# Kernel optimization log

Measured on AMD Instinct MI355X. Metric: run time of the kernel, lower is better.

The kernel has to match this reference:

```python
import jax, jax.numpy as jnp
import numpy as np

B, S = 64, 64
IMG_F, EMB, HID, VOCAB = 2048, 512, 512, 32000


def setup_inputs() -> dict:
    key = jax.random.key(0)
    ks = jax.random.split(key, 12)
    s = 0.02
    return {
        "img": jax.random.normal(ks[0], (B, IMG_F), jnp.float32),
        "captions": jax.random.randint(ks[1], (B, S), 0, VOCAB),
        "embed_W": jax.random.normal(ks[2], (VOCAB, EMB), jnp.float32) * s,
        "Wi": jax.random.normal(ks[3], (IMG_F, HID), jnp.float32) * s,
        "bi": jax.random.normal(ks[4], (HID,), jnp.float32) * s,
        "Wx": jax.random.normal(ks[5], (EMB, HID), jnp.float32) * s,
        "bx": jax.random.normal(ks[6], (HID,), jnp.float32) * s,
        "Wh": jax.random.normal(ks[7], (HID, HID), jnp.float32) * s,
        "bh": jax.random.normal(ks[8], (HID, HID)[:1] + (HID,), jnp.float32)[0] * s if False else jax.random.normal(ks[8], (HID,), jnp.float32) * s,
        "Wy": jax.random.normal(ks[9], (HID, VOCAB), jnp.float32) * s,
        "by": jax.random.normal(ks[10], (VOCAB,), jnp.float32) * s,
    }


def reference(img, captions, embed_W, Wi, bi, Wx, bx, Wh, bh, Wy, by):
    # Embed caption inputs (drop last token): (B, T, EMB), T = S-1
    x = embed_W[captions[:, :-1]]
    # Precompute input-to-hidden preactivations for all steps: (B, T, HID)
    pre = jnp.einsum("bte,eh->bth", x, Wx) + bx
    # Image features are injected only at t=0 (as in the torch loop)
    pre = pre.at[:, 0].add(img @ Wi + bi)

    def step(h_prev, p_t):
        h_t = jnp.tanh(p_t + h_prev @ Wh + bh)
        return h_t, h_t

    h0 = jnp.zeros((img.shape[0], Wh.shape[0]), dtype=x.dtype)
    _, hs = jax.lax.scan(step, h0, pre.transpose(1, 0, 2))  # (T, B, HID)
    hs = hs.transpose(1, 0, 2)  # (B, T, HID)
    # Output projection in one big GEMM (same math as per-step h2y)
    logits = jnp.einsum("bth,hv->btv", hs, Wy) + by  # (B, T, VOCAB)
    return logits
```

## Files before the change

kernel.cpp:

```cpp
#include <hip/hip_runtime.h>
#include <hip/hip_bf16.h>

#define B_    64
#define S_    64
#define T_    63
#define IMGF  2048
#define EMB   512
#define HID   512
#define VOCAB 32000
#define MROWS 4032
#define MPAD  4096

typedef __bf16 bf16;
typedef __bf16 bf16x8 __attribute__((ext_vector_type(8)));
typedef float  f32x4  __attribute__((ext_vector_type(4)));

__device__ __forceinline__ void gload_lds16(const void* g, void* l) {
  __builtin_amdgcn_global_load_lds(
      (const __attribute__((address_space(1))) unsigned int*)g,
      (__attribute__((address_space(3))) unsigned int*)l, 16, 0, 0);
}

__global__ __launch_bounds__(256) void transpose_w(
    const float* __restrict__ W, bf16* __restrict__ WT, int K, int N)
{
  __shared__ float tile[64][65];
  const int tx = threadIdx.x & 63, ty = threadIdx.x >> 6;
  const int n0 = blockIdx.x * 64, k0 = blockIdx.y * 64;
  #pragma unroll
  for (int r = ty; r < 64; r += 4)
    tile[r][tx] = W[(size_t)(k0 + r) * N + n0 + tx];
  __syncthreads();
  #pragma unroll
  for (int r = ty; r < 64; r += 4)
    WT[(size_t)(n0 + r) * K + k0 + tx] = (bf16)tile[tx][r];
}

__global__ __launch_bounds__(256) void embed_gather(
    const float* __restrict__ embW, const int* __restrict__ captions,
    bf16* __restrict__ X)
{
  const int r = blockIdx.x;
  const int tid = threadIdx.x;
  if (r < MROWS) {
    const int b = r / T_, t = r % T_;
    const int idx = captions[b * S_ + t];
    float2 v = ((const float2*)(embW + (size_t)idx * EMB))[tid];
    X[(size_t)r * EMB + 2 * tid]     = (bf16)v.x;
    X[(size_t)r * EMB + 2 * tid + 1] = (bf16)v.y;
  } else {
    X[(size_t)r * EMB + 2 * tid]     = (bf16)0.f;
    X[(size_t)r * EMB + 2 * tid + 1] = (bf16)0.f;
  }
}

__global__ __launch_bounds__(256) void img_to_bf16(
    const float* __restrict__ img, bf16* __restrict__ imgB)
{
  const int r = blockIdx.x;
  const int tid = threadIdx.x;
  #pragma unroll
  for (int j = 0; j < 8; j++) {
    const int c = tid + j * 256;
    const float v = (r < B_) ? img[(size_t)r * IMGF + c] : 0.f;
    imgB[(size_t)r * IMGF + c] = (bf16)v;
  }
}

__global__ __launch_bounds__(256) void gemm_bt(
    const bf16* __restrict__ A, const bf16* __restrict__ BT,
    const float* __restrict__ bias, float* __restrict__ C,
    int Mvalid, int N, int K)
{
  __shared__ __align__(16) bf16 As[128 * 32];
  __shared__ __align__(16) bf16 Bs[128 * 32];
  const int tid  = threadIdx.x;
  const int wave = tid >> 6, lane = tid & 63;
  const int wm = wave >> 1, wn = wave & 1;
  const int bn = blockIdx.x, bm = blockIdx.y;
  const int lg = lane >> 4, lr = lane & 15;

  f32x4 acc[4][4];
  #pragma unroll
  for (int m = 0; m < 4; m++)
    #pragma unroll
    for (int n = 0; n < 4; n++) acc[m][n] = (f32x4){0.f, 0.f, 0.f, 0.f};

  const bf16* Abase = A  + (size_t)bm * 128 * K;
  const bf16* Bbase = BT + (size_t)bn * 128 * K;

  for (int kt = 0; kt < K; kt += 32) {
    __syncthreads();
    #pragma unroll
    for (int i = 0; i < 2; i++) {
      const int c = i * 256 + wave * 64 + lane;
      const int r = c >> 2;
      const int sl = (c & 3) ^ ((r >> 1) & 3);
      gload_lds16(Abase + (size_t)r * K + kt + sl * 8,
                  &As[(i * 256 + wave * 64) * 8]);
    }
    #pragma unroll
    for (int i = 0; i < 2; i++) {
      const int c = i * 256 + wave * 64 + lane;
      const int r = c >> 2;
      const int sl = (c & 3) ^ ((r >> 1) & 3);
      gload_lds16(Bbase + (size_t)r * K + kt + sl * 8,
                  &Bs[(i * 256 + wave * 64) * 8]);
    }
    __syncthreads();

    bf16x8 af[4], bfr[4];
    #pragma unroll
    for (int m = 0; m < 4; m++) {
      const int r = wm * 64 + m * 16 + lr;
      const int sp = lg ^ ((r >> 1) & 3);
      af[m] = *(const bf16x8*)&As[r * 32 + sp * 8];
    }
    #pragma unroll
    for (int n = 0; n < 4; n++) {
      const int r = wn * 64 + n * 16 + lr;
      const int sp = lg ^ ((r >> 1) & 3);
      bfr[n] = *(const bf16x8*)&Bs[r * 32 + sp * 8];
    }
    #pragma unroll
    for (int m = 0; m < 4; m++)
      #pragma unroll
      for (int n = 0; n < 4; n++)
        acc[m][n] = __builtin_amdgcn_mfma_f32_16x16x32_bf16(af[m], bfr[n], acc[m][n], 0, 0, 0);
  }

  const int row0 = bm * 128 + wm * 64 + (lane >> 4) * 4;
  const int col0 = bn * 128 + wn * 64 + lr;
  #pragma unroll
  for (int m = 0; m < 4; m++) {
    #pragma unroll
    for (int n = 0; n < 4; n++) {
      const int col = col0 + n * 16;
      const float bv = bias[col];
      #pragma unroll
      for (int q = 0; q < 4; q++) {
        const int row = row0 + m * 16 + q;
        if (row < Mvalid) C[(size_t)row * N + col] = acc[m][n][q] + bv;
      }
    }
  }
}

#define FREG 47
#define FLDS 17
__global__ __launch_bounds__(512, 2) void rnn_reg8(
    const float* __restrict__ pre, const bf16* __restrict__ WhT,
    const float* __restrict__ bh, const float* __restrict__ pimg,
    bf16* __restrict__ hs)
{
  const int bg  = blockIdx.x;
  const int tid = threadIdx.x;
  const int wave = tid >> 6, lane = tid & 63;
  const int lg = lane >> 4, lr = lane & 15;
  const int gb0 = bg * 16;
  const int wc0 = wave * 64;

  __shared__ __align__(16) bf16 hsh[16 * 512];
  __shared__ __align__(16) bf16 bls[8 * FLDS * 64 * 8];

  bf16x8 bw[FREG];
  #pragma unroll
  for (int f = 0; f < 64; f++) {
    const int n = f >> 4, kf = f & 15;
    const bf16x8 v = *(const bf16x8*)(WhT + (size_t)(wc0 + n * 16 + lr) * 512
                                          + kf * 32 + lg * 8);
    if (f < FREG) bw[f] = v;
    else *(bf16x8*)&bls[((wave * FLDS + (f - FREG)) * 64 + lane) * 8] = v;
  }

  *(f32x4*)&hsh[tid * 16]     = (f32x4){0.f, 0.f, 0.f, 0.f};
  *(f32x4*)&hsh[tid * 16 + 8] = (f32x4){0.f, 0.f, 0.f, 0.f};

  float bhv[4];
  #pragma unroll
  for (int n = 0; n < 4; n++) bhv[n] = bh[wc0 + n * 16 + lr];
  const float* preb = pre + ((size_t)(gb0 + lg * 4) * T_) * 512 + wc0 + lr;

  __syncthreads();

  #pragma unroll 1
  for (int t = 0; t < T_; t++) {
    float prq[4][4];
    #pragma unroll
    for (int n = 0; n < 4; n++)
      #pragma unroll
      for (int q = 0; q < 4; q++)
        prq[n][q] = preb[(size_t)q * (T_ * 512) + (size_t)t * 512 + n * 16];

    f32x4 acc[4];
    #pragma unroll
    for (int n = 0; n < 4; n++) acc[n] = (f32x4){0.f, 0.f, 0.f, 0.f};

    #pragma unroll
    for (int kf = 0; kf < 16; kf++) {
      const int c = (kf * 4 + lg) ^ (lr & 7);
      const bf16x8 a = *(const bf16x8*)&hsh[(lr * 64 + c) * 8];
      #pragma unroll
      for (int n = 0; n < 4; n++) {
        const int f = n * 16 + kf;
        bf16x8 bfrag;
        if (f < FREG) bfrag = bw[f];
        else bfrag = *(const bf16x8*)&bls[((wave * FLDS + (f - FREG)) * 64 + lane) * 8];
        acc[n] = __builtin_amdgcn_mfma_f32_16x16x32_bf16(a, bfrag, acc[n], 0, 0, 0);
      }
    }
    __syncthreads();

    #pragma unroll
    for (int n = 0; n < 4; n++) {
      #pragma unroll
      for (int q = 0; q < 4; q++) {
        const int bl = lg * 4 + q;
        const int b  = gb0 + bl;
        const int k  = wc0 + n * 16 + lr;
        float s = acc[n][q] + prq[n][q] + bhv[n];
        if (t == 0) s += pimg[(size_t)b * HID + k];
        const float e = __builtin_exp2f(s * 2.885390081777927f);
        const float hv = 1.f - 2.f * __builtin_amdgcn_rcpf(e + 1.f);
        hs[((size_t)b * T_ + t) * HID + k] = (bf16)hv;
        const int c = (k >> 3) ^ (bl & 7);
        hsh[bl * 512 + c * 8 + (k & 7)] = (bf16)hv;
      }
    }
    __syncthreads();
  }
}

extern "C" void kernel_launch(void* const* d_in, const int* in_sizes, int n_in,
                              void* d_out, int out_size, void* d_ws, size_t ws_size,
                              hipStream_t stream) {
  const float* img      = (const float*)d_in[0];
  const int*   captions = (const int*)d_in[1];
  const float* embW     = (const float*)d_in[2];
  const float* Wi       = (const float*)d_in[3];
  const float* bi       = (const float*)d_in[4];
  const float* Wx       = (const float*)d_in[5];
  const float* bx       = (const float*)d_in[6];
  const float* Wh       = (const float*)d_in[7];
  const float* bh       = (const float*)d_in[8];
  const float* Wy       = (const float*)d_in[9];
  const float* by       = (const float*)d_in[10];
  float* logits = (float*)d_out;

  char* ws = (char*)d_ws;
  bf16*  WyT  = (bf16*)(ws);
  bf16*  WxT  = (bf16*)(ws + 32768000);
  bf16*  X    = (bf16*)(ws + 33292288);
  bf16*  hs   = (bf16*)(ws + 37486592);
  float* pre  = (float*)(ws + 41680896);
  float* pimg = (float*)(ws + 49938432);
  bf16*  imgB = (bf16*)(ws + 50200576);
  bf16*  WiT  = (bf16*)(ws + 50724864);
  bf16*  WhT  = WxT;

  transpose_w<<<dim3(VOCAB / 64, HID / 64), 256, 0, stream>>>(Wy, WyT, HID, VOCAB);
  transpose_w<<<dim3(HID / 64, EMB / 64), 256, 0, stream>>>(Wx, WxT, EMB, HID);
  transpose_w<<<dim3(HID / 64, IMGF / 64), 256, 0, stream>>>(Wi, WiT, IMGF, HID);
  img_to_bf16<<<128, 256, 0, stream>>>(img, imgB);

  embed_gather<<<MPAD, 256, 0, stream>>>(embW, captions, X);

  gemm_bt<<<dim3(HID / 128, MPAD / 128), 256, 0, stream>>>(X, WxT, bx, pre, MROWS, HID, HID);

  gemm_bt<<<dim3(HID / 128, 1), 256, 0, stream>>>(imgB, WiT, bi, pimg, B_, HID, IMGF);

  transpose_w<<<dim3(HID / 64, HID / 64), 256, 0, stream>>>(Wh, WhT, HID, HID);

  hipMemsetAsync(hs + (size_t)MROWS * HID, 0,
                 (size_t)(MPAD - MROWS) * HID * sizeof(bf16), stream);

  rnn_reg8<<<4, 512, 0, stream>>>(pre, WhT, bh, pimg, hs);

  gemm_bt<<<dim3(VOCAB / 128, MPAD / 128), 256, 0, stream>>>(hs, WyT, by, logits, MROWS, VOCAB, HID);
}
```

Baseline: 667.9 us.

## Double-buffer GEMM tiles, reorder grid, retune RNN register split and barriers

The GEMM now double-buffers its LDS tiles, issuing global-to-LDS loads for the next K tile before computing the current one, so there is one barrier per iteration instead of two. The grid mapping is swapped so blockIdx.x walks M, which changes which tiles share the weight panel in cache. The RNN kernel keeps one more weight fragment in registers (48 of 64), relaxes launch bounds to one block per CU, and replaces __syncthreads with an explicit lgkmcnt wait plus s_barrier. There is a correctness risk: the next tile's global_load_lds is issued right after the barrier while there is no vmcnt wait before the current buffer is read, so the code relies on the compiler inserting that wait.

```diff
diff --git a/kernel.cpp b/kernel.cpp
--- a/kernel.cpp
+++ b/kernel.cpp
@@ -20,6 +20,8 @@
       (const __attribute__((address_space(1))) unsigned int*)g,
       (__attribute__((address_space(3))) unsigned int*)l, 16, 0, 0);
 }
+
+#define LGKM_BARRIER() asm volatile("s_waitcnt lgkmcnt(0)\n\ts_barrier" ::: "memory")
 
 __global__ __launch_bounds__(256) void transpose_w(
     const float* __restrict__ W, bf16* __restrict__ WT, int K, int N)
@@ -72,12 +74,12 @@
     const float* __restrict__ bias, float* __restrict__ C,
     int Mvalid, int N, int K)
 {
-  __shared__ __align__(16) bf16 As[128 * 32];
-  __shared__ __align__(16) bf16 Bs[128 * 32];
+  __shared__ __align__(16) bf16 As[2][128 * 32];
+  __shared__ __align__(16) bf16 Bs[2][128 * 32];
   const int tid  = threadIdx.x;
   const int wave = tid >> 6, lane = tid & 63;
   const int wm = wave >> 1, wn = wave & 1;
-  const int bn = blockIdx.x, bm = blockIdx.y;
+  const int bm = blockIdx.x, bn = blockIdx.y;
   const int lg = lane >> 4, lr = lane & 15;
 
   f32x4 acc[4][4];
@@ -89,45 +91,52 @@
   const bf16* Abase = A  + (size_t)bm * 128 * K;
   const bf16* Bbase = BT + (size_t)bn * 128 * K;
 
-  for (int kt = 0; kt < K; kt += 32) {
+  const int c0 = wave * 64 + lane;
+  const int r0 = c0 >> 2,  sl0 = (c0 & 3) ^ ((r0 >> 1) & 3);
+  const int c1 = 256 + c0;
+  const int r1 = c1 >> 2,  sl1 = (c1 & 3) ^ ((r1 >> 1) & 3);
+
+  const int NT = K >> 5;
+
+#define STAGE_TILE(buf, kt)                                                   \
+  do {                                                                        \
+    gload_lds16(Abase + (size_t)r0 * K + (kt) + sl0 * 8,                      \
+                &As[buf][(wave * 64) * 8]);                                   \
+    gload_lds16(Abase + (size_t)r1 * K + (kt) + sl1 * 8,                      \
+                &As[buf][(256 + wave * 64) * 8]);                             \
+    gload_lds16(Bbase + (size_t)r0 * K + (kt) + sl0 * 8,                      \
+                &Bs[buf][(wave * 64) * 8]);                                   \
+    gload_lds16(Bbase + (size_t)r1 * K + (kt) + sl1 * 8,                      \
+                &Bs[buf][(256 + wave * 64) * 8]);                             \
+  } while (0)
+
+  STAGE_TILE(0, 0);
+  int cur = 0;
+  for (int it = 0; it < NT; ++it) {
     __syncthreads();
-    #pragma unroll
-    for (int i = 0; i < 2; i++) {
-      const int c = i * 256 + wave * 64 + lane;
-      const int r = c >> 2;
-      const int sl = (c & 3) ^ ((r >> 1) & 3);
-      gload_lds16(Abase + (size_t)r * K + kt + sl * 8,
-                  &As[(i * 256 + wave * 64) * 8]);
-    }
-    #pragma unroll
-    for (int i = 0; i < 2; i++) {
-      const int c = i * 256 + wave * 64 + lane;
-      const int r = c >> 2;
-      const int sl = (c & 3) ^ ((r >> 1) & 3);
-      gload_lds16(Bbase + (size_t)r * K + kt + sl * 8,
-                  &Bs[(i * 256 + wave * 64) * 8]);
-    }
-    __syncthreads();
+    if (it + 1 < NT) STAGE_TILE(cur ^ 1, (it + 1) * 32);
 
     bf16x8 af[4], bfr[4];
     #pragma unroll
     for (int m = 0; m < 4; m++) {
       const int r = wm * 64 + m * 16 + lr;
       const int sp = lg ^ ((r >> 1) & 3);
-      af[m] = *(const bf16x8*)&As[r * 32 + sp * 8];
+      af[m] = *(const bf16x8*)&As[cur][r * 32 + sp * 8];
     }
     #pragma unroll
     for (int n = 0; n < 4; n++) {
       const int r = wn * 64 + n * 16 + lr;
       const int sp = lg ^ ((r >> 1) & 3);
-      bfr[n] = *(const bf16x8*)&Bs[r * 32 + sp * 8];
+      bfr[n] = *(const bf16x8*)&Bs[cur][r * 32 + sp * 8];
     }
     #pragma unroll
     for (int m = 0; m < 4; m++)
       #pragma unroll
       for (int n = 0; n < 4; n++)
         acc[m][n] = __builtin_amdgcn_mfma_f32_16x16x32_bf16(af[m], bfr[n], acc[m][n], 0, 0, 0);
-  }
+    cur ^= 1;
+  }
+#undef STAGE_TILE
 
   const int row0 = bm * 128 + wm * 64 + (lane >> 4) * 4;
   const int col0 = bn * 128 + wn * 64 + lr;
@@ -146,9 +155,9 @@
   }
 }
 
-#define FREG 47
-#define FLDS 17
-__global__ __launch_bounds__(512, 2) void rnn_reg8(
+#define FREG 48
+#define FLDS 16
+__global__ __launch_bounds__(512, 1) void rnn_reg8(
     const float* __restrict__ pre, const bf16* __restrict__ WhT,
     const float* __restrict__ bh, const float* __restrict__ pimg,
     bf16* __restrict__ hs)
@@ -209,7 +218,7 @@
         acc[n] = __builtin_amdgcn_mfma_f32_16x16x32_bf16(a, bfrag, acc[n], 0, 0, 0);
       }
     }
-    __syncthreads();
+    LGKM_BARRIER();
 
     #pragma unroll
     for (int n = 0; n < 4; n++) {
@@ -227,7 +236,7 @@
         hsh[bl * 512 + c * 8 + (k & 7)] = (bf16)hv;
       }
     }
-    __syncthreads();
+    LGKM_BARRIER();
   }
 }
 
@@ -265,9 +274,9 @@
 
   embed_gather<<<MPAD, 256, 0, stream>>>(embW, captions, X);
 
-  gemm_bt<<<dim3(HID / 128, MPAD / 128), 256, 0, stream>>>(X, WxT, bx, pre, MROWS, HID, HID);
-
-  gemm_bt<<<dim3(HID / 128, 1), 256, 0, stream>>>(imgB, WiT, bi, pimg, B_, HID, IMGF);
+  gemm_bt<<<dim3(MPAD / 128, HID / 128), 256, 0, stream>>>(X, WxT, bx, pre, MROWS, HID, HID);
+
+  gemm_bt<<<dim3(1, HID / 128), 256, 0, stream>>>(imgB, WiT, bi, pimg, B_, HID, IMGF);
 
   transpose_w<<<dim3(HID / 64, HID / 64), 256, 0, stream>>>(Wh, WhT, HID, HID);
 
@@ -276,5 +285,5 @@
 
   rnn_reg8<<<4, 512, 0, stream>>>(pre, WhT, bh, pimg, hs);
 
-  gemm_bt<<<dim3(VOCAB / 128, MPAD / 128), 256, 0, stream>>>(hs, WyT, by, logits, MROWS, VOCAB, HID);
-}
+  gemm_bt<<<dim3(MPAD / 128, VOCAB / 128), 256, 0, stream>>>(hs, WyT, by, logits, MROWS, VOCAB, HID);
+}
```

Measured after the change: 679.9 us. Within noise of the previous version (+1.8%).
